# Performance work log

Hardware: AMD Instinct MI355X
Metric: run time of the kernel (lower is better)

Reference implementation:

```python
import jax, jax.numpy as jnp
import numpy as np

SIGMA2 = 0.01       # inlier_params[0] -> Scorer_dist sigma2
INLIER_ALPHA = 0.5  # inlier_params[-1]


def setup_inputs() -> dict:
    key = jax.random.key(0)
    k1, k2, k3 = jax.random.split(key, 3)
    B, H, N = 32, 256, 8192
    pts = jax.random.normal(k1, (B, N, 3), dtype=jnp.float32)
    target = jax.random.normal(k2, (B, 3), dtype=jnp.float32)
    sample_idx = jax.random.randint(k3, (B, H, 3), 0, N)
    return {"pts": pts, "target": target, "sample_idx": sample_idx}


def _fit_planes(pts, sample_idx):
    # gather 3 points per hypothesis: pts [B,N,3], sample_idx [B,H,3] -> [B,H,3,3]
    B = pts.shape[0]
    b_idx = jnp.arange(B)[:, None, None]
    tri = pts[b_idx, sample_idx]                     # [B,H,3pts,3coords]
    p0, p1, p2 = tri[:, :, 0], tri[:, :, 1], tri[:, :, 2]
    n = jnp.cross(p1 - p0, p2 - p0)                  # plane normal [B,H,3]
    d = -jnp.sum(n * p0, axis=-1, keepdims=True)     # plane offset [B,H,1]
    planes = jnp.concatenate([n, d], axis=-1)        # [B,H,4]
    # sample_hyp fallback: degenerate (all-zero) planes replaced by ones
    all_zero = jnp.all(planes == 0, axis=-1, keepdims=True)
    planes = jnp.where(all_zero, jnp.ones_like(planes), planes)
    # normalize all 4 components by normal norm
    norm = jnp.sqrt(jnp.sum(planes[..., :3] ** 2, axis=-1, keepdims=True))
    return planes / norm


def reference(pts, target, sample_idx):
    B = pts.shape[0]
    planes = _fit_planes(pts, sample_idx)            # [B,H,4]
    normal = planes[..., :3]
    # Scorer_dist: |n . p + d| over all points, gaussian, sum over points
    dists = jnp.abs(jnp.einsum('bhc,bnc->bhn', normal, pts) + planes[..., 3:4])
    score = jnp.sum(jnp.exp(-(dists ** 2) / (2.0 * SIGMA2)), axis=2)  # [B,H]
    # ms_euclidean loss against target normal (sign-invariant)
    t = target[:, None, :]                           # [B,1,3]
    loss = jnp.minimum(jnp.sum((normal - t) ** 2, axis=2),
                       jnp.sum((normal + t) ** 2, axis=2))            # [B,H]
    maxidx = jnp.argmax(score, axis=1)               # [B]
    top_loss = jnp.take_along_axis(loss, maxidx[:, None], axis=1)[:, 0]
    pred = jnp.take_along_axis(normal, maxidx[:, None, None], axis=1)[:, 0]
    w = jax.nn.softmax(INLIER_ALPHA * score, axis=1)
    exp_loss = jnp.sum(loss * w, axis=1)             # [B]
    return exp_loss, top_loss, pred
```

## Files before the change

### kernel.cpp

```cpp
#include <hip/hip_runtime.h>
#include <math.h>

#define BB 32
#define HH 256
#define NN 8192
#define CC 32
#define CHUNK (NN / CC)
#define P 8
#define SUB (CHUNK / P)

#define WS_LOSS_F ((size_t)BB * HH * 4)
#define WS_PART_F (WS_LOSS_F + (size_t)BB * HH)

__global__ __launch_bounds__(HH) void score_kernel(
    const float* __restrict__ pts, const float* __restrict__ target,
    const int* __restrict__ sidx, float* __restrict__ ws,
    float* __restrict__ partial) {
  const int chunk = blockIdx.x, b = blockIdx.y;
  const int h = threadIdx.x;
  __shared__ float4 smp[CHUNK * 3 / 4];
  __shared__ float4 plane_lds[HH];
  __shared__ float scorepad[HH * 9];

  const float4* src4 =
      (const float4*)(pts + ((long)b * NN + (long)chunk * CHUNK) * 3);
  if (h < CHUNK * 3 / 4) {
    __builtin_amdgcn_global_load_lds(src4 + h, &smp[h], 16, 0, 0);
  }

  long ibase = ((long)b * HH + h) * 3;
  int i0 = sidx[ibase], i1 = sidx[ibase + 1], i2 = sidx[ibase + 2];
  const float* pb = pts + (long)b * NN * 3;
  float p0x = pb[3 * i0], p0y = pb[3 * i0 + 1], p0z = pb[3 * i0 + 2];
  float p1x = pb[3 * i1], p1y = pb[3 * i1 + 1], p1z = pb[3 * i1 + 2];
  float p2x = pb[3 * i2], p2y = pb[3 * i2 + 1], p2z = pb[3 * i2 + 2];
  float v1x = p1x - p0x, v1y = p1y - p0y, v1z = p1z - p0z;
  float v2x = p2x - p0x, v2y = p2y - p0y, v2z = p2z - p0z;
  float nx = __fsub_rn(__fmul_rn(v1y, v2z), __fmul_rn(v1z, v2y));
  float ny = __fsub_rn(__fmul_rn(v1z, v2x), __fmul_rn(v1x, v2z));
  float nz = __fsub_rn(__fmul_rn(v1x, v2y), __fmul_rn(v1y, v2x));
  float d = -(__fmul_rn(nx, p0x) + __fmul_rn(ny, p0y) + __fmul_rn(nz, p0z));
  if (nx == 0.0f && ny == 0.0f && nz == 0.0f && d == 0.0f) {
    nx = 1.0f; ny = 1.0f; nz = 1.0f; d = 1.0f;
  }
  float norm = sqrtf(nx * nx + ny * ny + nz * nz);
  nx /= norm; ny /= norm; nz /= norm; d /= norm;
  plane_lds[h] = make_float4(nx, ny, nz, d);

  if (chunk == 0) {
    ((float4*)ws)[b * HH + h] = make_float4(nx, ny, nz, d);
    float tx = target[b * 3], ty = target[b * 3 + 1], tz = target[b * 3 + 2];
    float lm = (nx - tx) * (nx - tx) + (ny - ty) * (ny - ty) + (nz - tz) * (nz - tz);
    float lp = (nx + tx) * (nx + tx) + (ny + ty) * (ny + ty) + (nz + tz) * (nz + tz);
    ws[WS_LOSS_F + b * HH + h] = fminf(lm, lp);
  }
  __syncthreads();

  const float SC = 8.4932180028801371f;
  const int pid = h & 31;
  const int s = h >> 5;
  float4 pls[P];
#pragma unroll
  for (int k = 0; k < P; ++k) {
    float4 q = plane_lds[pid + (k << 5)];
    pls[k] = make_float4(q.x * SC, q.y * SC, q.z * SC, q.w * SC);
  }

  float acc[P];
#pragma unroll
  for (int k = 0; k < P; ++k) acc[k] = 0.f;
  const int sbase = s * (SUB * 3 / 4);
#pragma unroll 2
  for (int g = 0; g < SUB / 4; ++g) {
    float4 v0 = smp[sbase + 3 * g + 0];
    float4 v1 = smp[sbase + 3 * g + 1];
    float4 v2 = smp[sbase + 3 * g + 2];
#pragma unroll
    for (int k = 0; k < P; ++k) {
      float4 q = pls[k];
      float t0 = fmaf(q.x, v0.x, fmaf(q.y, v0.y, fmaf(q.z, v0.z, q.w)));
      float t1 = fmaf(q.x, v0.w, fmaf(q.y, v1.x, fmaf(q.z, v1.y, q.w)));
      float t2 = fmaf(q.x, v1.z, fmaf(q.y, v1.w, fmaf(q.z, v2.x, q.w)));
      float t3 = fmaf(q.x, v2.y, fmaf(q.y, v2.z, fmaf(q.z, v2.w, q.w)));
      float e0 = __builtin_amdgcn_exp2f(-(t0 * t0));
      float e1 = __builtin_amdgcn_exp2f(-(t1 * t1));
      float e2 = __builtin_amdgcn_exp2f(-(t2 * t2));
      float e3 = __builtin_amdgcn_exp2f(-(t3 * t3));
      acc[k] += (e0 + e1) + (e2 + e3);
    }
  }

#pragma unroll
  for (int k = 0; k < P; ++k) scorepad[(pid + (k << 5)) * 9 + s] = acc[k];
  __syncthreads();
  float rowsum = 0.f;
#pragma unroll
  for (int j = 0; j < P; ++j) rowsum += scorepad[h * 9 + j];
  partial[((long)b * CC + chunk) * HH + h] = rowsum;
}

__global__ __launch_bounds__(HH) void finalize_kernel(
    const float* __restrict__ ws, float* __restrict__ out) {
  int b = blockIdx.x, h = threadIdx.x;
  const float* lossArr = ws + WS_LOSS_F;
  const float* partial = ws + WS_PART_F;
  float s = 0.f;
#pragma unroll
  for (int c = 0; c < CC; ++c) s += partial[((long)b * CC + c) * HH + h];
  float l = lossArr[b * HH + h];

  __shared__ float sv[HH];
  __shared__ int si[HH];
  __shared__ float s1[HH];
  __shared__ float s2[HH];
  sv[h] = s; si[h] = h;
  __syncthreads();
  for (int off = HH / 2; off > 0; off >>= 1) {
    if (h < off) {
      float o = sv[h + off]; int oi = si[h + off];
      if (o > sv[h] || (o == sv[h] && oi < si[h])) { sv[h] = o; si[h] = oi; }
    }
    __syncthreads();
  }
  float m = sv[0];
  int mi = si[0];
  __syncthreads();
  const float HL = 0.72134752044448170f;
  float wv = __builtin_amdgcn_exp2f(HL * (s - m));
  s1[h] = wv; s2[h] = wv * l;
  __syncthreads();
  for (int off = HH / 2; off > 0; off >>= 1) {
    if (h < off) { s1[h] += s1[h + off]; s2[h] += s2[h + off]; }
    __syncthreads();
  }
  if (h == 0) {
    out[b] = s2[0] / s1[0];
    out[BB + b] = lossArr[b * HH + mi];
    float4 p = ((const float4*)ws)[b * HH + mi];
    out[2 * BB + b * 3 + 0] = p.x;
    out[2 * BB + b * 3 + 1] = p.y;
    out[2 * BB + b * 3 + 2] = p.z;
  }
}

extern "C" void kernel_launch(void* const* d_in, const int* in_sizes, int n_in,
                              void* d_out, int out_size, void* d_ws, size_t ws_size,
                              hipStream_t stream) {
  const float* pts = (const float*)d_in[0];
  const float* target = (const float*)d_in[1];
  const int* sidx = (const int*)d_in[2];
  float* out = (float*)d_out;
  float* ws = (float*)d_ws;
  float* partial = ws + WS_PART_F;

  score_kernel<<<dim3(CC, BB), HH, 0, stream>>>(pts, target, sidx, ws, partial);
  finalize_kernel<<<BB, HH, 0, stream>>>(ws, out);
}
```

Baseline: 23.67 us.

## Halve chunk count, deepen unroll, and use wavefront shuffles in finalize

Cuts the number of point chunks per batch from 32 to 16, so each score block processes twice as many points and the per-block plane fitting and partial-sum traffic are amortized over more work. The LDS staging load becomes a strided loop to cover the larger chunk, and the inner loop unroll rises from 2 to 4. The finalize kernel replaces its shared-memory tree reductions (argmax and softmax sums) with wavefront xor-shuffles plus a 4-entry cross-wave combine, reducing barriers. Fewer blocks (512) lowers parallelism on the GPU and doubles LDS use per block, which may hurt occupancy.

```diff
diff --git a/kernel.cpp b/kernel.cpp
--- a/kernel.cpp
+++ b/kernel.cpp
@@ -4,7 +4,7 @@
 #define BB 32
 #define HH 256
 #define NN 8192
-#define CC 32
+#define CC 16
 #define CHUNK (NN / CC)
 #define P 8
 #define SUB (CHUNK / P)
@@ -24,8 +24,9 @@
 
   const float4* src4 =
       (const float4*)(pts + ((long)b * NN + (long)chunk * CHUNK) * 3);
-  if (h < CHUNK * 3 / 4) {
-    __builtin_amdgcn_global_load_lds(src4 + h, &smp[h], 16, 0, 0);
+#pragma unroll
+  for (int j = h; j < CHUNK * 3 / 4; j += HH) {
+    __builtin_amdgcn_global_load_lds(src4 + j, &smp[j], 16, 0, 0);
   }
 
   long ibase = ((long)b * HH + h) * 3;
@@ -70,7 +71,7 @@
 #pragma unroll
   for (int k = 0; k < P; ++k) acc[k] = 0.f;
   const int sbase = s * (SUB * 3 / 4);
-#pragma unroll 2
+#pragma unroll 4
   for (int g = 0; g < SUB / 4; ++g) {
     float4 v0 = smp[sbase + 3 * g + 0];
     float4 v1 = smp[sbase + 3 * g + 1];
@@ -109,37 +110,46 @@
   for (int c = 0; c < CC; ++c) s += partial[((long)b * CC + c) * HH + h];
   float l = lossArr[b * HH + h];
 
-  __shared__ float sv[HH];
-  __shared__ int si[HH];
-  __shared__ float s1[HH];
-  __shared__ float s2[HH];
-  sv[h] = s; si[h] = h;
+  __shared__ float redv[4];
+  __shared__ int redi[4];
+  __shared__ float sw[4], swl[4];
+
+  float v = s; int idx = h;
+#pragma unroll
+  for (int o = 32; o > 0; o >>= 1) {
+    float ov = __shfl_xor(v, o);
+    int oi = __shfl_xor(idx, o);
+    if (ov > v || (ov == v && oi < idx)) { v = ov; idx = oi; }
+  }
+  const int wid = h >> 6;
+  if ((h & 63) == 0) { redv[wid] = v; redi[wid] = idx; }
   __syncthreads();
-  for (int off = HH / 2; off > 0; off >>= 1) {
-    if (h < off) {
-      float o = sv[h + off]; int oi = si[h + off];
-      if (o > sv[h] || (o == sv[h] && oi < si[h])) { sv[h] = o; si[h] = oi; }
-    }
-    __syncthreads();
+  float m = redv[0]; int mi = redi[0];
+#pragma unroll
+  for (int w = 1; w < 4; ++w) {
+    float ov = redv[w]; int oi = redi[w];
+    if (ov > m || (ov == m && oi < mi)) { m = ov; mi = oi; }
   }
-  float m = sv[0];
-  int mi = si[0];
-  __syncthreads();
+
   const float HL = 0.72134752044448170f;
   float wv = __builtin_amdgcn_exp2f(HL * (s - m));
-  s1[h] = wv; s2[h] = wv * l;
+  float wl = wv * l;
+#pragma unroll
+  for (int o = 32; o > 0; o >>= 1) {
+    wv += __shfl_xor(wv, o);
+    wl += __shfl_xor(wl, o);
+  }
+  if ((h & 63) == 0) { sw[wid] = wv; swl[wid] = wl; }
   __syncthreads();
-  for (int off = HH / 2; off > 0; off >>= 1) {
-    if (h < off) { s1[h] += s1[h + off]; s2[h] += s2[h + off]; }
-    __syncthreads();
-  }
   if (h == 0) {
-    out[b] = s2[0] / s1[0];
+    float S1 = (sw[0] + sw[1]) + (sw[2] + sw[3]);
+    float S2 = (swl[0] + swl[1]) + (swl[2] + swl[3]);
+    out[b] = S2 / S1;
     out[BB + b] = lossArr[b * HH + mi];
     float4 p = ((const float4*)ws)[b * HH + mi];
-    out[2 * BB + b * 3 + 0] = p.x;
-    out[2 * BB + b * 3 + 1] = p.y;
-    out[2 * BB + b * 3 + 2] = p.z;
+    out[2 * BB + 3 * b + 0] = p.x;
+    out[2 * BB + 3 * b + 1] = p.y;
+    out[2 * BB + 3 * b + 2] = p.z;
   }
 }
 
```

Result: faster. 22.95 us (-3.1%).
